# Optimization experiments

Hardware: AMD Instinct MI355X
Metric: run time of the kernel (lower is better)

The kernel has to match this reference:

```python
import jax, jax.numpy as jnp
import numpy as np

N_NODES = 50000
N_EDGES = 800000
IN_CH = 128
HID = 16
HEADS = 8
OUT_CH = 40
NEG_SLOPE = 0.2  # PyG GATConv default leaky_relu slope


def segment_softmax(logits, seg, num_segments):
    # logits: [E, H], softmax over edges sharing the same destination node
    m = jax.ops.segment_max(logits, seg, num_segments=num_segments)  # [N, H]
    e = jnp.exp(logits - m[seg])
    s = jax.ops.segment_sum(e, seg, num_segments=num_segments)  # [N, H]
    return e / s[seg]


def gat_conv(x, edge_index, W, att_src, att_dst, bias, heads, ch, concat):
    N = x.shape[0]
    h = (x @ W).reshape(N, heads, ch)                     # [N, H, C]
    a_src = jnp.sum(h * att_src, axis=-1)                 # [N, H]
    a_dst = jnp.sum(h * att_dst, axis=-1)                 # [N, H]
    src, dst = edge_index[0], edge_index[1]
    alpha = jax.nn.leaky_relu(a_src[src] + a_dst[dst], NEG_SLOPE)  # [E, H]
    alpha = segment_softmax(alpha, dst, N)                # [E, H]
    msg = h[src] * alpha[:, :, None]                      # [E, H, C]
    out = jax.ops.segment_sum(msg, dst, num_segments=N)   # [N, H, C]
    out = out.reshape(N, heads * ch) if concat else out.mean(axis=1)
    return out + bias


def setup_inputs() -> dict:
    key = jax.random.key(0)
    ks = jax.random.split(key, 10)
    g = 0.1
    return {
        "x": jax.random.normal(ks[0], (N_NODES, IN_CH), jnp.float32),
        "edge_index": jax.random.randint(ks[1], (2, N_EDGES), 0, N_NODES, jnp.int32),
        "W1": jax.random.normal(ks[2], (IN_CH, HEADS * HID), jnp.float32) * g,
        "att_src1": jax.random.normal(ks[3], (HEADS, HID), jnp.float32) * g,
        "att_dst1": jax.random.normal(ks[4], (HEADS, HID), jnp.float32) * g,
        "b1": jnp.zeros((HEADS * HID,), jnp.float32),
        "W2": jax.random.normal(ks[5], (HEADS * HID, OUT_CH), jnp.float32) * g,
        "att_src2": jax.random.normal(ks[6], (1, OUT_CH), jnp.float32) * g,
        "att_dst2": jax.random.normal(ks[7], (1, OUT_CH), jnp.float32) * g,
        "b2": jnp.zeros((OUT_CH,), jnp.float32),
    }


def reference(x, edge_index, W1, att_src1, att_dst1, b1, W2, att_src2, att_dst2, b2):
    # layer 1: GATConv(in->hid, heads=8, concat) + ELU (dropout is identity in eval)
    h = gat_conv(x, edge_index, W1, att_src1, att_dst1, b1, HEADS, HID, concat=True)
    h = jax.nn.elu(h)
    # layer 2: GATConv(hid*heads->out, heads=1, concat=False)
    out = gat_conv(h, edge_index, W2, att_src2, att_dst2, b2, 1, OUT_CH, concat=False)
    return out
```

## Files before the change

kernel.cpp:

```cpp
#include <hip/hip_runtime.h>
#include <hip/hip_bf16.h>
#include <math.h>

#define N_NODES 50000
#define E_EDGES 800000
#define IN_CH 128
#define HIDX 128
#define OUT_CH 40
#define NEG_SLOPE 0.2f
#define RANK_BLKS 160
#define EDGES_PER_RANK_BLK 5000
#define GEMM_BLKS_X 782
#define PAD_SHIFT 6
#define POISON_I ((int)0xAAAAAAAA)

static __device__ __forceinline__ unsigned int f2bf_pk(float lo, float hi) {
    unsigned int ul = __float_as_uint(lo);
    unsigned int uh = __float_as_uint(hi);
    ul = (ul + 0x7fffu + ((ul >> 16) & 1u)) >> 16;
    uh = (uh + 0x7fffu + ((uh >> 16) & 1u)) >> 16;
    return ul | (uh << 16);
}
static __device__ __forceinline__ float bf2f(unsigned short u) {
    return __uint_as_float(((unsigned int)u) << 16);
}


__global__ __launch_bounds__(256) void gemm1_kernel(
    const float* __restrict__ x, const float* __restrict__ W1,
    const float* __restrict__ as1, const float* __restrict__ ad1,
    unsigned short* __restrict__ H1, float* __restrict__ A1s, float* __restrict__ A1d,
    const int* __restrict__ ei, int* __restrict__ deg, unsigned short* __restrict__ csr_pad)
{
    int tid = threadIdx.x;
    int bid = blockIdx.x;

    if (bid < RANK_BLKS) {
        int start = bid * EDGES_PER_RANK_BLK;
        int endv  = start + EDGES_PER_RANK_BLK;
        if (endv > E_EDGES) endv = E_EDGES;
        for (int base = start; base < endv; base += 1024) {
            int e0 = base + tid;
            int e1 = e0 + 256, e2 = e0 + 512, e3 = e0 + 768;
            bool v0 = e0 < endv, v1 = e1 < endv, v2 = e2 < endv, v3 = e3 < endv;
            int d0 = 0, d1 = 0, d2 = 0, d3 = 0;
            int s0 = 0, s1 = 0, s2 = 0, s3 = 0;
            if (v0) { d0 = ei[E_EDGES + e0]; s0 = ei[e0]; }
            if (v1) { d1 = ei[E_EDGES + e1]; s1 = ei[e1]; }
            if (v2) { d2 = ei[E_EDGES + e2]; s2 = ei[e2]; }
            if (v3) { d3 = ei[E_EDGES + e3]; s3 = ei[e3]; }
            int r0, r1, r2, r3;
            if (v0) r0 = atomicAdd(&deg[d0], 1) - POISON_I;
            if (v1) r1 = atomicAdd(&deg[d1], 1) - POISON_I;
            if (v2) r2 = atomicAdd(&deg[d2], 1) - POISON_I;
            if (v3) r3 = atomicAdd(&deg[d3], 1) - POISON_I;
            if (v0) csr_pad[(d0 << PAD_SHIFT) + r0] = (unsigned short)s0;
            if (v1) csr_pad[(d1 << PAD_SHIFT) + r1] = (unsigned short)s1;
            if (v2) csr_pad[(d2 << PAD_SHIFT) + r2] = (unsigned short)s2;
            if (v3) csr_pad[(d3 << PAD_SHIFT) + r3] = (unsigned short)s3;
        }
        return;
    }

    __shared__ float Ws[64 * 68];
    __shared__ float XT[64 * 68];
    int g = bid - RANK_BLKS;
    int rowbase = (g >> 1) * 64;
    int cb = g & 1;

    const float4* W4 = (const float4*)W1;
    const float4* x4 = (const float4*)x;

    int cg = tid & 15;
    int rg = tid >> 4;
    int c0 = cg * 4;
    int r0 = rg * 4;
    float acc[4][4];
#pragma unroll
    for (int i = 0; i < 4; i++)
#pragma unroll
        for (int j = 0; j < 4; j++) acc[i][j] = 0.f;

#pragma unroll
    for (int kh = 0; kh < 2; kh++) {
        if (kh) __syncthreads();
#pragma unroll
        for (int i = 0; i < 4; i++) {
            int f = i * 256 + tid;
            int k = f >> 4, c4 = f & 15;
            *(float4*)(Ws + k * 68 + c4 * 4) = W4[(kh * 64 + k) * 32 + cb * 16 + c4];
        }
#pragma unroll
        for (int i = 0; i < 4; i++) {
            int f = i * 256 + tid;
            int r = f >> 4, c4 = f & 15;
            int gr = rowbase + r; if (gr >= N_NODES) gr = N_NODES - 1;
            *(float4*)(XT + r * 68 + c4 * 4) = x4[gr * 32 + kh * 16 + c4];
        }
        __syncthreads();

        for (int k = 0; k < 64; k += 4) {
            float4 xv[4];
#pragma unroll
            for (int i = 0; i < 4; i++) xv[i] = *(const float4*)(XT + (r0 + i) * 68 + k);
#pragma unroll
            for (int kk = 0; kk < 4; kk++) {
                float4 wv = *(const float4*)(Ws + (k + kk) * 68 + c0);
#pragma unroll
                for (int i = 0; i < 4; i++) {
                    float xs = (kk == 0) ? xv[i].x : (kk == 1) ? xv[i].y : (kk == 2) ? xv[i].z : xv[i].w;
                    acc[i][0] += xs * wv.x; acc[i][1] += xs * wv.y;
                    acc[i][2] += xs * wv.z; acc[i][3] += xs * wv.w;
                }
            }
        }
    }

    int gc0 = cb * 64 + c0;
    int hh = gc0 >> 4;
    float asp[4] = {0, 0, 0, 0}, adp[4] = {0, 0, 0, 0};
#pragma unroll
    for (int j = 0; j < 4; j++) {
        float va = as1[gc0 + j];
        float vd = ad1[gc0 + j];
#pragma unroll
        for (int i = 0; i < 4; i++) { asp[i] += acc[i][j] * va; adp[i] += acc[i][j] * vd; }
    }
#pragma unroll
    for (int i = 0; i < 4; i++) {
        asp[i] += __shfl_xor(asp[i], 1); asp[i] += __shfl_xor(asp[i], 2);
        adp[i] += __shfl_xor(adp[i], 1); adp[i] += __shfl_xor(adp[i], 2);
    }
#pragma unroll
    for (int i = 0; i < 4; i++) {
        int gr = rowbase + r0 + i;
        if (gr < N_NODES) {
            uint2 v;
            v.x = f2bf_pk(acc[i][0], acc[i][1]);
            v.y = f2bf_pk(acc[i][2], acc[i][3]);
            *(uint2*)(H1 + gr * 128 + gc0) = v;
            if ((cg & 3) == 0) {
                A1s[gr * 8 + hh] = asp[i];
                A1d[gr * 8 + hh] = adp[i];
            }
        }
    }
}


__global__ __launch_bounds__(256) void agg1_kernel(
    const int* __restrict__ deg, const unsigned short* __restrict__ csr_pad,
    const float* __restrict__ A1s, const float* __restrict__ A1d,
    const unsigned short* __restrict__ H1, const float* __restrict__ b1,
    unsigned short* __restrict__ X2)
{
    int gwave = (blockIdx.x * blockDim.x + threadIdx.x) >> 6;
    int lane = threadIdx.x & 63;
    if (gwave >= N_NODES) return;
    int node = gwave;
    int beg = node << PAD_SHIFT;
    int end = beg + (deg[node] - POISON_I);
    int half = lane >> 5;
    int li = lane & 31;
    int head = li >> 2;
    int c0 = li * 4;
    float ad = A1d[node * 8 + head];
    float acc0 = 0.f, acc1 = 0.f, acc2 = 0.f, acc3 = 0.f, sumw = 0.f;
    for (int p = beg; p < end; p += 16) {
        int s[8]; float a[8]; ushort4 u[8]; bool v[8];
#pragma unroll
        for (int t = 0; t < 8; t++) {
            int e = p + 2 * t + half;
            v[t] = e < end;
            s[t] = csr_pad[v[t] ? e : beg];
        }
#pragma unroll
        for (int t = 0; t < 8; t++) a[t] = A1s[s[t] * 8 + head];
#pragma unroll
        for (int t = 0; t < 8; t++) u[t] = *(const ushort4*)(H1 + s[t] * 128 + c0);
#pragma unroll
        for (int t = 0; t < 8; t++) {
            float z = a[t] + ad; z = z >= 0.f ? z : NEG_SLOPE * z;
            float w = v[t] ? __expf(z) : 0.f;
            acc0 += w * bf2f(u[t].x);
            acc1 += w * bf2f(u[t].y);
            acc2 += w * bf2f(u[t].z);
            acc3 += w * bf2f(u[t].w);
            sumw += w;
        }
    }
    acc0 += __shfl_xor(acc0, 32);
    acc1 += __shfl_xor(acc1, 32);
    acc2 += __shfl_xor(acc2, 32);
    acc3 += __shfl_xor(acc3, 32);
    sumw += __shfl_xor(sumw, 32);
    if (half == 0) {
        float inv = (end > beg) ? 1.0f / sumw : 0.0f;
        float4 bv = *(const float4*)(b1 + c0);
        float o0 = acc0 * inv + bv.x;
        float o1 = acc1 * inv + bv.y;
        float o2 = acc2 * inv + bv.z;
        float o3 = acc3 * inv + bv.w;
        o0 = o0 > 0.f ? o0 : expm1f(o0);
        o1 = o1 > 0.f ? o1 : expm1f(o1);
        o2 = o2 > 0.f ? o2 : expm1f(o2);
        o3 = o3 > 0.f ? o3 : expm1f(o3);
        uint2 ov;
        ov.x = f2bf_pk(o0, o1);
        ov.y = f2bf_pk(o2, o3);
        *(uint2*)(X2 + node * 128 + c0) = ov;
    }
}


__global__ __launch_bounds__(256) void gemm2_kernel(
    const unsigned short* __restrict__ X2, const float* __restrict__ W2,
    const float* __restrict__ as2, const float* __restrict__ ad2,
    unsigned short* __restrict__ H2, float* __restrict__ A2s, float* __restrict__ A2d)
{
    __shared__ float Ws[128 * 40];
    __shared__ float XS[64 * 132];
    int tid = threadIdx.x;
    int rowbase = blockIdx.x * 64;

#pragma unroll
    for (int i = 0; i < 20; i++) Ws[i * 256 + tid] = W2[i * 256 + tid];

    const uint2* x2v = (const uint2*)X2;
#pragma unroll
    for (int i = 0; i < 8; i++) {
        int f = i * 256 + tid;
        int r = f >> 5, c4 = f & 31;
        int gr = rowbase + r; if (gr >= N_NODES) gr = N_NODES - 1;
        uint2 pk = x2v[gr * 32 + c4];
        float* dst = XS + r * 132 + c4 * 4;
        dst[0] = bf2f((unsigned short)(pk.x & 0xffff));
        dst[1] = bf2f((unsigned short)(pk.x >> 16));
        dst[2] = bf2f((unsigned short)(pk.y & 0xffff));
        dst[3] = bf2f((unsigned short)(pk.y >> 16));
    }
    __syncthreads();

    int q = tid & 3, r = tid >> 2;
    float acc[10];
#pragma unroll
    for (int j = 0; j < 10; j++) acc[j] = 0.f;
    for (int k = 0; k < 128; k += 4) {
        float4 xv = *(const float4*)(XS + r * 132 + k);
#pragma unroll
        for (int kk = 0; kk < 4; kk++) {
            float xs = (kk == 0) ? xv.x : (kk == 1) ? xv.y : (kk == 2) ? xv.z : xv.w;
#pragma unroll
            for (int j = 0; j < 10; j++) acc[j] += xs * Ws[(k + kk) * 40 + q * 10 + j];
        }
    }
    float asum = 0.f, dsum = 0.f;
#pragma unroll
    for (int j = 0; j < 10; j++) {
        asum += acc[j] * as2[q * 10 + j];
        dsum += acc[j] * ad2[q * 10 + j];
    }
    asum += __shfl_xor(asum, 1); asum += __shfl_xor(asum, 2);
    dsum += __shfl_xor(dsum, 1); dsum += __shfl_xor(dsum, 2);
    int gr = rowbase + r;
    if (gr < N_NODES) {
#pragma unroll
        for (int t = 0; t < 5; t++)
            *(unsigned int*)(H2 + gr * 40 + q * 10 + t * 2) = f2bf_pk(acc[t * 2], acc[t * 2 + 1]);
        if (q == 0) { A2s[gr] = asum; A2d[gr] = dsum; }
    }
}


__global__ __launch_bounds__(256) void agg2_kernel(
    const int* __restrict__ deg, const unsigned short* __restrict__ csr_pad,
    const float* __restrict__ A2s, const float* __restrict__ A2d,
    const unsigned short* __restrict__ H2, const float* __restrict__ b2,
    float* __restrict__ out)
{
    int gwave = (blockIdx.x * blockDim.x + threadIdx.x) >> 6;
    int lane = threadIdx.x & 63;
    if (gwave >= N_NODES) return;
    int node = gwave;
    int beg = node << PAD_SHIFT;
    int end = beg + (deg[node] - POISON_I);
    int half = lane >> 5;
    int li = lane & 31;
    bool act = li < 20;
    int c0 = li * 2;
    int cc = act ? c0 : 0;
    float ad = A2d[node];
    float acc0 = 0.f, acc1 = 0.f, sumw = 0.f;
    for (int p = beg; p < end; p += 16) {
        int s[8]; float a[8]; ushort2 u[8]; bool v[8];
#pragma unroll
        for (int t = 0; t < 8; t++) {
            int e = p + 2 * t + half;
            v[t] = e < end;
            s[t] = csr_pad[v[t] ? e : beg];
        }
#pragma unroll
        for (int t = 0; t < 8; t++) a[t] = A2s[s[t]];
#pragma unroll
        for (int t = 0; t < 8; t++) u[t] = *(const ushort2*)(H2 + s[t] * OUT_CH + cc);
#pragma unroll
        for (int t = 0; t < 8; t++) {
            float z = a[t] + ad; z = z >= 0.f ? z : NEG_SLOPE * z;
            float w = v[t] ? __expf(z) : 0.f;
            acc0 += w * bf2f(u[t].x);
            acc1 += w * bf2f(u[t].y);
            sumw += w;
        }
    }
    acc0 += __shfl_xor(acc0, 32);
    acc1 += __shfl_xor(acc1, 32);
    sumw += __shfl_xor(sumw, 32);
    if (half == 0 && act) {
        float inv = (end > beg) ? 1.0f / sumw : 0.0f;
        float o0 = acc0 * inv + b2[c0];
        float o1 = acc1 * inv + b2[c0 + 1];
        float2 ov = {o0, o1};
        *(float2*)(out + node * OUT_CH + c0) = ov;
    }
}


extern "C" void kernel_launch(void* const* d_in, const int* in_sizes, int n_in,
                              void* d_out, int out_size, void* d_ws, size_t ws_size,
                              hipStream_t stream) {
    const float* x   = (const float*)d_in[0];
    const int*   ei  = (const int*)d_in[1];
    const float* W1  = (const float*)d_in[2];
    const float* as1 = (const float*)d_in[3];
    const float* ad1 = (const float*)d_in[4];
    const float* b1  = (const float*)d_in[5];
    const float* W2  = (const float*)d_in[6];
    const float* as2 = (const float*)d_in[7];
    const float* ad2 = (const float*)d_in[8];
    const float* b2  = (const float*)d_in[9];
    float* out = (float*)d_out;

    char* ws = (char*)d_ws;
    size_t off = 0;
    auto alloc = [&](size_t bytes) {
        void* p = ws + off;
        off += (bytes + 255) & ~size_t(255);
        return p;
    };
    unsigned short* H1 = (unsigned short*)alloc((size_t)N_NODES * 128 * 2);
    unsigned short* X2 = (unsigned short*)alloc((size_t)N_NODES * 128 * 2);
    unsigned short* H2 = (unsigned short*)alloc((size_t)N_NODES * OUT_CH * 2);
    float* A1s    = (float*)alloc((size_t)N_NODES * 8 * 4);
    float* A1d    = (float*)alloc((size_t)N_NODES * 8 * 4);
    float* A2s    = (float*)alloc((size_t)N_NODES * 4);
    float* A2d    = (float*)alloc((size_t)N_NODES * 4);
    int* deg      = (int*)alloc((size_t)N_NODES * 4);
    unsigned short* csr_pad = (unsigned short*)alloc((size_t)N_NODES * 64 * 2);


    gemm1_kernel<<<RANK_BLKS + GEMM_BLKS_X * 2, 256, 0, stream>>>(
        x, W1, as1, ad1, H1, A1s, A1d, ei, deg, csr_pad);

    agg1_kernel<<<(N_NODES + 3) / 4, 256, 0, stream>>>(deg, csr_pad, A1s, A1d, H1, b1, X2);

    gemm2_kernel<<<(N_NODES + 63) / 64, 256, 0, stream>>>(X2, W2, as2, ad2, H2, A2s, A2d);
    agg2_kernel<<<(N_NODES + 3) / 4, 256, 0, stream>>>(deg, csr_pad, A2s, A2d, H2, b2, out);
}
```

Before: 219.8 us.

## Fuse layer-2 linear transform and attention projections into agg1 kernel

Removes the separate gemm2 kernel and the X2 intermediate buffer. Each wave now writes its ELU output row into shared memory and computes the 40-column H2 row, plus the A2s/A2d attention scores, directly with per-lane dot products over W2 read from global memory. This saves one launch and a 12.8MB bf16 write and read round-trip. In exchange each node does a 128x40 matvec with no W2 reuse through shared memory, using only 40 of 64 lanes. There is no __syncthreads, but it is not needed because each wave reads only its own shared row, and lanes of one wave execute together.

```diff
diff --git a/kernel.cpp b/kernel.cpp
--- a/kernel.cpp
+++ b/kernel.cpp
@@ -20,6 +20,10 @@
     ul = (ul + 0x7fffu + ((ul >> 16) & 1u)) >> 16;
     uh = (uh + 0x7fffu + ((uh >> 16) & 1u)) >> 16;
     return ul | (uh << 16);
+}
+static __device__ __forceinline__ unsigned short f2bf1(float v) {
+    unsigned int u = __float_as_uint(v);
+    return (unsigned short)((u + 0x7fffu + ((u >> 16) & 1u)) >> 16);
 }
 static __device__ __forceinline__ float bf2f(unsigned short u) {
     return __uint_as_float(((unsigned int)u) << 16);
@@ -152,8 +156,12 @@
     const int* __restrict__ deg, const unsigned short* __restrict__ csr_pad,
     const float* __restrict__ A1s, const float* __restrict__ A1d,
     const unsigned short* __restrict__ H1, const float* __restrict__ b1,
-    unsigned short* __restrict__ X2)
+    const float* __restrict__ W2, const float* __restrict__ as2,
+    const float* __restrict__ ad2,
+    unsigned short* __restrict__ H2, float* __restrict__ A2s, float* __restrict__ A2d)
 {
+    __shared__ float x2s[4][132];
+    int wid = threadIdx.x >> 6;
     int gwave = (blockIdx.x * blockDim.x + threadIdx.x) >> 6;
     int lane = threadIdx.x & 63;
     if (gwave >= N_NODES) return;
@@ -205,70 +213,25 @@
         o1 = o1 > 0.f ? o1 : expm1f(o1);
         o2 = o2 > 0.f ? o2 : expm1f(o2);
         o3 = o3 > 0.f ? o3 : expm1f(o3);
-        uint2 ov;
-        ov.x = f2bf_pk(o0, o1);
-        ov.y = f2bf_pk(o2, o3);
-        *(uint2*)(X2 + node * 128 + c0) = ov;
-    }
-}
-
-
-__global__ __launch_bounds__(256) void gemm2_kernel(
-    const unsigned short* __restrict__ X2, const float* __restrict__ W2,
-    const float* __restrict__ as2, const float* __restrict__ ad2,
-    unsigned short* __restrict__ H2, float* __restrict__ A2s, float* __restrict__ A2d)
-{
-    __shared__ float Ws[128 * 40];
-    __shared__ float XS[64 * 132];
-    int tid = threadIdx.x;
-    int rowbase = blockIdx.x * 64;
-
-#pragma unroll
-    for (int i = 0; i < 20; i++) Ws[i * 256 + tid] = W2[i * 256 + tid];
-
-    const uint2* x2v = (const uint2*)X2;
-#pragma unroll
-    for (int i = 0; i < 8; i++) {
-        int f = i * 256 + tid;
-        int r = f >> 5, c4 = f & 31;
-        int gr = rowbase + r; if (gr >= N_NODES) gr = N_NODES - 1;
-        uint2 pk = x2v[gr * 32 + c4];
-        float* dst = XS + r * 132 + c4 * 4;
-        dst[0] = bf2f((unsigned short)(pk.x & 0xffff));
-        dst[1] = bf2f((unsigned short)(pk.x >> 16));
-        dst[2] = bf2f((unsigned short)(pk.y & 0xffff));
-        dst[3] = bf2f((unsigned short)(pk.y >> 16));
-    }
-    __syncthreads();
-
-    int q = tid & 3, r = tid >> 2;
-    float acc[10];
-#pragma unroll
-    for (int j = 0; j < 10; j++) acc[j] = 0.f;
-    for (int k = 0; k < 128; k += 4) {
-        float4 xv = *(const float4*)(XS + r * 132 + k);
-#pragma unroll
-        for (int kk = 0; kk < 4; kk++) {
-            float xs = (kk == 0) ? xv.x : (kk == 1) ? xv.y : (kk == 2) ? xv.z : xv.w;
-#pragma unroll
-            for (int j = 0; j < 10; j++) acc[j] += xs * Ws[(k + kk) * 40 + q * 10 + j];
-        }
-    }
-    float asum = 0.f, dsum = 0.f;
-#pragma unroll
-    for (int j = 0; j < 10; j++) {
-        asum += acc[j] * as2[q * 10 + j];
-        dsum += acc[j] * ad2[q * 10 + j];
-    }
-    asum += __shfl_xor(asum, 1); asum += __shfl_xor(asum, 2);
-    dsum += __shfl_xor(dsum, 1); dsum += __shfl_xor(dsum, 2);
-    int gr = rowbase + r;
-    if (gr < N_NODES) {
-#pragma unroll
-        for (int t = 0; t < 5; t++)
-            *(unsigned int*)(H2 + gr * 40 + q * 10 + t * 2) = f2bf_pk(acc[t * 2], acc[t * 2 + 1]);
-        if (q == 0) { A2s[gr] = asum; A2d[gr] = dsum; }
-    }
+        float4 ov = {o0, o1, o2, o3};
+        *(float4*)(&x2s[wid][c0]) = ov;
+    }
+    float h2 = 0.f;
+    int c = lane;
+    if (c < OUT_CH) {
+#pragma unroll 8
+        for (int k = 0; k < 128; k++)
+            h2 += x2s[wid][k] * W2[k * OUT_CH + c];
+    }
+    float asv = (c < OUT_CH) ? h2 * as2[c] : 0.f;
+    float adv = (c < OUT_CH) ? h2 * ad2[c] : 0.f;
+#pragma unroll
+    for (int off = 1; off < 64; off <<= 1) {
+        asv += __shfl_xor(asv, off);
+        adv += __shfl_xor(adv, off);
+    }
+    if (c < OUT_CH) H2[node * OUT_CH + c] = f2bf1(h2);
+    if (lane == 0) { A2s[node] = asv; A2d[node] = adv; }
 }
 
 
@@ -348,7 +311,6 @@
         return p;
     };
     unsigned short* H1 = (unsigned short*)alloc((size_t)N_NODES * 128 * 2);
-    unsigned short* X2 = (unsigned short*)alloc((size_t)N_NODES * 128 * 2);
     unsigned short* H2 = (unsigned short*)alloc((size_t)N_NODES * OUT_CH * 2);
     float* A1s    = (float*)alloc((size_t)N_NODES * 8 * 4);
     float* A1d    = (float*)alloc((size_t)N_NODES * 8 * 4);
@@ -361,8 +323,8 @@
     gemm1_kernel<<<RANK_BLKS + GEMM_BLKS_X * 2, 256, 0, stream>>>(
         x, W1, as1, ad1, H1, A1s, A1d, ei, deg, csr_pad);
 
-    agg1_kernel<<<(N_NODES + 3) / 4, 256, 0, stream>>>(deg, csr_pad, A1s, A1d, H1, b1, X2);
-
-    gemm2_kernel<<<(N_NODES + 63) / 64, 256, 0, stream>>>(X2, W2, as2, ad2, H2, A2s, A2d);
+    agg1_kernel<<<(N_NODES + 3) / 4, 256, 0, stream>>>(
+        deg, csr_pad, A1s, A1d, H1, b1, W2, as2, ad2, H2, A2s, A2d);
+
     agg2_kernel<<<(N_NODES + 3) / 4, 256, 0, stream>>>(deg, csr_pad, A2s, A2d, H2, b2, out);
 }
```

Result: slower. 237.8 us (+8.2%).

## Compute layer-1 GEMM with bf16 MFMA using split-precision hi/lo operands

Applied to the files above, without the earlier changes.

Replaces the FP32 scalar-FMA register-tiled GEMM for x@W1 with MFMA 16x16x32 bf16 instructions. Each operand is split into a bf16 high part and a bf16 residual, and three MFMAs per tile (hi*hi, lo*hi, hi*lo) approximate FP32 accuracy. The epilogue is rewritten for the MFMA output layout, with wider shuffle reductions for the attention dot products and scalar bf16 stores to H1. This adds conversion work while staging into shared memory and narrower output stores. The GEMM is only one part of a kernel that also does CSR building and is followed by aggregation kernels.

```diff
diff --git a/kernel.cpp b/kernel.cpp
--- a/kernel.cpp
+++ b/kernel.cpp
@@ -14,12 +14,19 @@
 #define PAD_SHIFT 6
 #define POISON_I ((int)0xAAAAAAAA)
 
+typedef __attribute__((ext_vector_type(8))) short bf16x8;
+typedef __attribute__((ext_vector_type(4))) float f32x4;
+
 static __device__ __forceinline__ unsigned int f2bf_pk(float lo, float hi) {
     unsigned int ul = __float_as_uint(lo);
     unsigned int uh = __float_as_uint(hi);
     ul = (ul + 0x7fffu + ((ul >> 16) & 1u)) >> 16;
     uh = (uh + 0x7fffu + ((uh >> 16) & 1u)) >> 16;
     return ul | (uh << 16);
+}
+static __device__ __forceinline__ unsigned short f2bf1(float v) {
+    unsigned int u = __float_as_uint(v);
+    return (unsigned short)((u + 0x7fffu + ((u >> 16) & 1u)) >> 16);
 }
 static __device__ __forceinline__ float bf2f(unsigned short u) {
     return __uint_as_float(((unsigned int)u) << 16);
@@ -62,89 +69,105 @@
         return;
     }
 
-    __shared__ float Ws[64 * 68];
-    __shared__ float XT[64 * 68];
+    __shared__ __align__(16) unsigned short XsH[64 * 80];
+    __shared__ __align__(16) unsigned short XsL[64 * 80];
+    __shared__ __align__(16) unsigned short WsH[64 * 80];
+    __shared__ __align__(16) unsigned short WsL[64 * 80];
     int g = bid - RANK_BLKS;
     int rowbase = (g >> 1) * 64;
     int cb = g & 1;
-
-    const float4* W4 = (const float4*)W1;
+    int lane = tid & 63;
+    int w = tid >> 6;
+    int rL = lane & 15;
+    int gq = lane >> 4;
+
+    f32x4 zero4 = {0.f, 0.f, 0.f, 0.f};
+    f32x4 acc0 = zero4, acc1 = zero4, acc2 = zero4, acc3 = zero4;
+
     const float4* x4 = (const float4*)x;
 
-    int cg = tid & 15;
-    int rg = tid >> 4;
-    int c0 = cg * 4;
-    int r0 = rg * 4;
-    float acc[4][4];
-#pragma unroll
-    for (int i = 0; i < 4; i++)
-#pragma unroll
-        for (int j = 0; j < 4; j++) acc[i][j] = 0.f;
+#define CT_STEP(ACC, CT) { \
+    const bf16x8 bH = *(const bf16x8*)(WsH + ((CT)*16 + rL)*80 + kb + gq*8); \
+    const bf16x8 bL = *(const bf16x8*)(WsL + ((CT)*16 + rL)*80 + kb + gq*8); \
+    ACC = __builtin_amdgcn_mfma_f32_16x16x32_bf16(aH, bH, ACC, 0, 0, 0); \
+    ACC = __builtin_amdgcn_mfma_f32_16x16x32_bf16(aL, bH, ACC, 0, 0, 0); \
+    ACC = __builtin_amdgcn_mfma_f32_16x16x32_bf16(aH, bL, ACC, 0, 0, 0); }
 
 #pragma unroll
     for (int kh = 0; kh < 2; kh++) {
         if (kh) __syncthreads();
-#pragma unroll
-        for (int i = 0; i < 4; i++) {
-            int f = i * 256 + tid;
-            int k = f >> 4, c4 = f & 15;
-            *(float4*)(Ws + k * 68 + c4 * 4) = W4[(kh * 64 + k) * 32 + cb * 16 + c4];
-        }
 #pragma unroll
         for (int i = 0; i < 4; i++) {
             int f = i * 256 + tid;
             int r = f >> 4, c4 = f & 15;
             int gr = rowbase + r; if (gr >= N_NODES) gr = N_NODES - 1;
-            *(float4*)(XT + r * 68 + c4 * 4) = x4[gr * 32 + kh * 16 + c4];
+            float4 v = x4[gr * 32 + kh * 16 + c4];
+            unsigned int h01 = f2bf_pk(v.x, v.y);
+            unsigned int h23 = f2bf_pk(v.z, v.w);
+            float rx = v.x - bf2f((unsigned short)(h01 & 0xffff));
+            float ry = v.y - bf2f((unsigned short)(h01 >> 16));
+            float rz = v.z - bf2f((unsigned short)(h23 & 0xffff));
+            float rw = v.w - bf2f((unsigned short)(h23 >> 16));
+            uint2 hv; hv.x = h01; hv.y = h23;
+            uint2 lv; lv.x = f2bf_pk(rx, ry); lv.y = f2bf_pk(rz, rw);
+            *(uint2*)(XsH + r * 80 + c4 * 4) = hv;
+            *(uint2*)(XsL + r * 80 + c4 * 4) = lv;
+        }
+        {
+            int wc = tid & 63;
+            int ks = tid >> 6;
+            const float* Wp = W1 + (kh * 64 + ks * 16) * 128 + cb * 64 + wc;
+            float wv[16];
+#pragma unroll
+            for (int i = 0; i < 16; i++) wv[i] = Wp[i * 128];
+#pragma unroll
+            for (int j2 = 0; j2 < 4; j2++) {
+                unsigned int h0 = f2bf_pk(wv[4 * j2], wv[4 * j2 + 1]);
+                unsigned int h1 = f2bf_pk(wv[4 * j2 + 2], wv[4 * j2 + 3]);
+                float q0 = wv[4 * j2]     - bf2f((unsigned short)(h0 & 0xffff));
+                float q1 = wv[4 * j2 + 1] - bf2f((unsigned short)(h0 >> 16));
+                float q2 = wv[4 * j2 + 2] - bf2f((unsigned short)(h1 & 0xffff));
+                float q3 = wv[4 * j2 + 3] - bf2f((unsigned short)(h1 >> 16));
+                uint2 hv; hv.x = h0; hv.y = h1;
+                uint2 lv; lv.x = f2bf_pk(q0, q1); lv.y = f2bf_pk(q2, q3);
+                *(uint2*)(WsH + wc * 80 + ks * 16 + j2 * 4) = hv;
+                *(uint2*)(WsL + wc * 80 + ks * 16 + j2 * 4) = lv;
+            }
         }
         __syncthreads();
-
-        for (int k = 0; k < 64; k += 4) {
-            float4 xv[4];
-#pragma unroll
-            for (int i = 0; i < 4; i++) xv[i] = *(const float4*)(XT + (r0 + i) * 68 + k);
-#pragma unroll
-            for (int kk = 0; kk < 4; kk++) {
-                float4 wv = *(const float4*)(Ws + (k + kk) * 68 + c0);
-#pragma unroll
-                for (int i = 0; i < 4; i++) {
-                    float xs = (kk == 0) ? xv[i].x : (kk == 1) ? xv[i].y : (kk == 2) ? xv[i].z : xv[i].w;
-                    acc[i][0] += xs * wv.x; acc[i][1] += xs * wv.y;
-                    acc[i][2] += xs * wv.z; acc[i][3] += xs * wv.w;
-                }
-            }
-        }
-    }
-
-    int gc0 = cb * 64 + c0;
-    int hh = gc0 >> 4;
-    float asp[4] = {0, 0, 0, 0}, adp[4] = {0, 0, 0, 0};
-#pragma unroll
-    for (int j = 0; j < 4; j++) {
-        float va = as1[gc0 + j];
-        float vd = ad1[gc0 + j];
-#pragma unroll
-        for (int i = 0; i < 4; i++) { asp[i] += acc[i][j] * va; adp[i] += acc[i][j] * vd; }
-    }
-#pragma unroll
-    for (int i = 0; i < 4; i++) {
-        asp[i] += __shfl_xor(asp[i], 1); asp[i] += __shfl_xor(asp[i], 2);
-        adp[i] += __shfl_xor(adp[i], 1); adp[i] += __shfl_xor(adp[i], 2);
-    }
-#pragma unroll
-    for (int i = 0; i < 4; i++) {
-        int gr = rowbase + r0 + i;
-        if (gr < N_NODES) {
-            uint2 v;
-            v.x = f2bf_pk(acc[i][0], acc[i][1]);
-            v.y = f2bf_pk(acc[i][2], acc[i][3]);
-            *(uint2*)(H1 + gr * 128 + gc0) = v;
-            if ((cg & 3) == 0) {
-                A1s[gr * 8 + hh] = asp[i];
-                A1d[gr * 8 + hh] = adp[i];
-            }
-        }
-    }
+#pragma unroll
+        for (int chunk = 0; chunk < 2; chunk++) {
+            int kb = chunk * 32;
+            int abase = (w * 16 + rL) * 80 + kb + gq * 8;
+            bf16x8 aH = *(const bf16x8*)(XsH + abase);
+            bf16x8 aL = *(const bf16x8*)(XsL + abase);
+            CT_STEP(acc0, 0)
+            CT_STEP(acc1, 1)
+            CT_STEP(acc2, 2)
+            CT_STEP(acc3, 3)
+        }
+    }
+#undef CT_STEP
+
+    int gr0 = rowbase + w * 16 + gq * 4;
+#define CT_EPI(ACC, CT) { \
+    float av = as1[cb * 64 + (CT) * 16 + rL]; \
+    float dv = ad1[cb * 64 + (CT) * 16 + rL]; \
+    _Pragma("unroll") \
+    for (int reg = 0; reg < 4; reg++) { \
+        float sv = ACC[reg] * av, dd = ACC[reg] * dv; \
+        sv += __shfl_xor(sv, 1); sv += __shfl_xor(sv, 2); sv += __shfl_xor(sv, 4); sv += __shfl_xor(sv, 8); \
+        dd += __shfl_xor(dd, 1); dd += __shfl_xor(dd, 2); dd += __shfl_xor(dd, 4); dd += __shfl_xor(dd, 8); \
+        int grr = gr0 + reg; \
+        if (grr < N_NODES) { \
+            H1[grr * 128 + cb * 64 + (CT) * 16 + rL] = f2bf1(ACC[reg]); \
+            if (rL == 0) { A1s[grr * 8 + cb * 4 + (CT)] = sv; A1d[grr * 8 + cb * 4 + (CT)] = dd; } \
+        } } }
+    CT_EPI(acc0, 0)
+    CT_EPI(acc1, 1)
+    CT_EPI(acc2, 2)
+    CT_EPI(acc3, 3)
+#undef CT_EPI
 }
 
 
```

Measured after the change: 220.1 us. About the same (+0.2%).
